# Kernel optimization log

Measured on AMD Instinct MI355X. Metric: run time of the kernel, lower is better.

The kernel has to match this reference:

```python
import jax, jax.numpy as jnp
import numpy as np

B, L, E, F = 4096, 200, 128, 64
NU = NI = 100000

def setup_inputs() -> dict:
    key = jax.random.key(0)
    ks = jax.random.split(key, 8)
    return {
        "user_ids": jax.random.randint(ks[0], (B,), 0, NU),
        "item_ids": jax.random.randint(ks[1], (B, L), 0, NI),
        "features": jax.random.normal(ks[2], (B, L, F), dtype=jnp.float32),
        "user_emb": jax.random.normal(ks[3], (NU, E), dtype=jnp.float32) * 0.1,
        "item_emb": jax.random.normal(ks[4], (NI, E), dtype=jnp.float32) * 0.1,
        "feat_w1": jax.random.normal(ks[5], (E, E + F), dtype=jnp.float32) * (2.0 / (E + F)) ** 0.5,
        "feat_b1": jnp.zeros((E,), jnp.float32),
        "feat_w2": jax.random.normal(ks[6], (E, E), dtype=jnp.float32) * (2.0 / E) ** 0.5,
        "feat_b2": jnp.zeros((E,), jnp.float32),
        "w1": jax.random.normal(ks[7], (E, 3 * E), dtype=jnp.float32) * (2.0 / (3 * E)) ** 0.5,
        "b1": jnp.zeros((E,), jnp.float32),
        "w2": jax.random.normal(jax.random.fold_in(key, 99), (1, E), dtype=jnp.float32) * (2.0 / E) ** 0.5,
        "b2": jnp.zeros((1,), jnp.float32),
    }

def reference(user_ids, item_ids, features, user_emb, item_emb,
              feat_w1, feat_b1, feat_w2, feat_b2, w1, b1, w2, b2):
    user = user_emb[user_ids]                      # [B, E]
    items = item_emb[item_ids]                     # [B, L, E]
    usern = jnp.broadcast_to(user[:, None, :], items.shape)  # [B, L, E]
    # FeatureNet: concat(user, features) -> Linear -> relu -> Linear -> relu
    fx = jnp.concatenate([usern, features], axis=-1)           # [B, L, E+F]
    fx = jax.nn.relu(jnp.einsum('blf,ef->ble', fx, feat_w1) + feat_b1)
    comp = jax.nn.relu(jnp.einsum('ble,oe->blo', fx, feat_w2) + feat_b2)  # [B, L, E]
    # attention MLP over concat(user, item, comp)
    x = jnp.concatenate([usern, items, comp], axis=-1)         # [B, L, 3E]
    x = jax.nn.relu(jnp.einsum('blf,ef->ble', x, w1) + b1)
    logits = jnp.einsum('ble,oe->blo', x, w2) + b2             # [B, L, 1]
    attn = jax.nn.softmax(logits, axis=1)                      # softmax over items
    out = user + jnp.sum(items * attn, axis=1)                 # [B, E]
    return out
```

## Files before the change

kernel.cpp:

```cpp
#include <hip/hip_runtime.h>
#include <math.h>

#define BB 4096
#define LL 200
#define EE 128
#define FF 64
#define NTHREADS 512

#define PITCH_F  72
#define PITCH_FX 136
#define PITCH_X3 264

typedef __attribute__((ext_vector_type(4))) float  floatx4;
typedef __attribute__((ext_vector_type(8))) short  shortx8;

#define MFMA16(a, b, c) __builtin_amdgcn_mfma_f32_16x16x32_bf16((a), (b), (c), 0, 0, 0)

__device__ __forceinline__ unsigned short f2bf(float f) {
    union { float f; unsigned u; } c; c.f = f;
    return (unsigned short)((c.u + 0x7fffu + ((c.u >> 16) & 1u)) >> 16);
}

__device__ __forceinline__ shortx8 load_bfrag(const float* p) {
    float4 v0 = ((const float4*)p)[0];
    float4 v1 = ((const float4*)p)[1];
    shortx8 r;
    r[0] = (short)f2bf(v0.x); r[1] = (short)f2bf(v0.y);
    r[2] = (short)f2bf(v0.z); r[3] = (short)f2bf(v0.w);
    r[4] = (short)f2bf(v1.x); r[5] = (short)f2bf(v1.y);
    r[6] = (short)f2bf(v1.z); r[7] = (short)f2bf(v1.w);
    return r;
}

__device__ __forceinline__ float waveMax(float v) {
    #pragma unroll
    for (int off = 32; off > 0; off >>= 1)
        v = fmaxf(v, __shfl_xor(v, off, 64));
    return v;
}
__device__ __forceinline__ float waveSum(float v) {
    #pragma unroll
    for (int off = 32; off > 0; off >>= 1)
        v += __shfl_xor(v, off, 64);
    return v;
}

__global__ __launch_bounds__(NTHREADS, 4)
void usernet_mfma(const int* __restrict__ user_ids,
                  const int* __restrict__ item_ids,
                  const float* __restrict__ features,
                  const float* __restrict__ user_emb,
                  const float* __restrict__ item_emb,
                  const float* __restrict__ feat_w1,
                  const float* __restrict__ feat_b1,
                  const float* __restrict__ feat_w2,
                  const float* __restrict__ feat_b2,
                  const float* __restrict__ w1,
                  const float* __restrict__ b1,
                  const float* __restrict__ w2,
                  const float* __restrict__ b2,
                  float* __restrict__ out)
{
    __shared__ __align__(16) unsigned short s_feat[64 * PITCH_F];
    __shared__ __align__(16) unsigned short s_fx  [64 * PITCH_FX];
    __shared__ __align__(16) unsigned short s_x3  [64 * PITCH_X3];
    __shared__ float s_user[EE];
    __shared__ float s_bias1[EE];
    __shared__ float s_bias2[EE];
    __shared__ float s_bias3[EE];
    __shared__ float s_w2[EE];
    __shared__ float s_lp[8][208];
    __shared__ float s_attn[208];
    __shared__ float s_red[12];
    __shared__ float s_part[4][EE];

    const int b    = blockIdx.x;
    const int tid  = threadIdx.x;
    const int lane = tid & 63;
    const int wv   = tid >> 6;
    const int m    = lane & 15;
    const int q    = lane >> 4;
    const int n0   = wv * 16 + m;

    shortx8 B1[2];
    shortx8 B2[4];
    shortx8 B3[8];
    #pragma unroll
    for (int ks = 0; ks < 2; ++ks)
        B1[ks] = load_bfrag(feat_w1 + (size_t)n0 * (EE + FF) + EE + ks * 32 + q * 8);
    #pragma unroll
    for (int ks = 0; ks < 4; ++ks)
        B2[ks] = load_bfrag(feat_w2 + (size_t)n0 * EE + ks * 32 + q * 8);
    #pragma unroll
    for (int ks = 0; ks < 8; ++ks)
        B3[ks] = load_bfrag(w1 + (size_t)n0 * (3 * EE) + EE + ks * 32 + q * 8);

    if (tid < 32) {
        const int uid = user_ids[b];
        ((float4*)s_user)[tid] = ((const float4*)(user_emb + (size_t)uid * EE))[tid];
    }
    if (tid >= 64 && tid < 64 + EE) {
        s_bias2[tid - 64] = feat_b2[tid - 64];
        s_w2[tid - 64]    = w2[tid - 64];
    }
    __syncthreads();

    if (tid < 256) {
        const int e    = tid & (EE - 1);
        const int half = tid >> 7;
        const float* wrow = half ? (w1 + (size_t)e * (3 * EE))
                                 : (feat_w1 + (size_t)e * (EE + FF));
        float acc = 0.f;
        #pragma unroll 8
        for (int k = 0; k < EE; ++k) acc += wrow[k] * s_user[k];
        if (half == 0) s_bias1[e] = acc + feat_b1[e];
        else           s_bias3[e] = acc + b1[e];
    }
    __syncthreads();

    const float bias1_0 = s_bias1[n0];
    const float bias2_0 = s_bias2[n0];
    const float bias3_0 = s_bias3[n0];
    const float w2_0    = s_w2[n0];

    for (int ch = 0; ch < 4; ++ch) {
        const int row0 = ch * 64;
        const int ntl  = (ch < 3) ? 4 : 1;
        const int rows = ntl * 16;

        for (int idx = tid; idx < rows * 16; idx += NTHREADS) {
            const int r = idx >> 4, c4 = idx & 15;
            const int l = row0 + r;
            float4 v = make_float4(0.f, 0.f, 0.f, 0.f);
            if (l < LL) v = ((const float4*)features)[((size_t)b * LL + l) * 16 + c4];
            ushort4 o; o.x = f2bf(v.x); o.y = f2bf(v.y); o.z = f2bf(v.z); o.w = f2bf(v.w);
            *(ushort4*)&s_feat[r * PITCH_F + c4 * 4] = o;
        }
        for (int idx = tid; idx < rows * 32; idx += NTHREADS) {
            const int r = idx >> 5, c4 = idx & 31;
            const int l = row0 + r;
            float4 v = make_float4(0.f, 0.f, 0.f, 0.f);
            if (l < LL) {
                const int id = item_ids[(size_t)b * LL + l];
                v = ((const float4*)item_emb)[(size_t)id * 32 + c4];
            }
            ushort4 o; o.x = f2bf(v.x); o.y = f2bf(v.y); o.z = f2bf(v.z); o.w = f2bf(v.w);
            *(ushort4*)&s_x3[r * PITCH_X3 + c4 * 4] = o;
        }
        __syncthreads();

        for (int mt = 0; mt < ntl; ++mt) {
            floatx4 a0 = {0.f, 0.f, 0.f, 0.f};
            const unsigned short* ap = s_feat + (mt * 16 + m) * PITCH_F + q * 8;
            #pragma unroll
            for (int ks = 0; ks < 2; ++ks) {
                shortx8 af = *(const shortx8*)(ap + ks * 32);
                a0 = MFMA16(af, B1[ks], a0);
            }
            #pragma unroll
            for (int r = 0; r < 4; ++r) {
                const int row = mt * 16 + q * 4 + r;
                float v0 = a0[r] + bias1_0; v0 = v0 > 0.f ? v0 : 0.f;
                s_fx[row * PITCH_FX + n0] = f2bf(v0);
            }
        }
        __syncthreads();

        for (int mt = 0; mt < ntl; ++mt) {
            floatx4 a0 = {0.f, 0.f, 0.f, 0.f};
            const unsigned short* ap = s_fx + (mt * 16 + m) * PITCH_FX + q * 8;
            #pragma unroll
            for (int ks = 0; ks < 4; ++ks) {
                shortx8 af = *(const shortx8*)(ap + ks * 32);
                a0 = MFMA16(af, B2[ks], a0);
            }
            #pragma unroll
            for (int r = 0; r < 4; ++r) {
                const int row = mt * 16 + q * 4 + r;
                float v0 = a0[r] + bias2_0; v0 = v0 > 0.f ? v0 : 0.f;
                s_x3[row * PITCH_X3 + EE + n0] = f2bf(v0);
            }
        }
        __syncthreads();

        for (int mt = 0; mt < ntl; ++mt) {
            floatx4 a0 = {0.f, 0.f, 0.f, 0.f};
            const unsigned short* ap = s_x3 + (mt * 16 + m) * PITCH_X3 + q * 8;
            #pragma unroll
            for (int ks = 0; ks < 8; ++ks) {
                shortx8 af = *(const shortx8*)(ap + ks * 32);
                a0 = MFMA16(af, B3[ks], a0);
            }
            #pragma unroll
            for (int r = 0; r < 4; ++r) {
                float v0 = a0[r] + bias3_0; v0 = v0 > 0.f ? v0 : 0.f;
                float p = v0 * w2_0;
                p += __shfl_xor(p, 1, 64);
                p += __shfl_xor(p, 2, 64);
                p += __shfl_xor(p, 4, 64);
                p += __shfl_xor(p, 8, 64);
                if (m == 0) s_lp[wv][row0 + mt * 16 + q * 4 + r] = p;
            }
        }
        __syncthreads();
    }

    const int wid = tid >> 6;
    float lv = -INFINITY;
    if (tid < LL) {
        lv = b2[0];
        #pragma unroll
        for (int w = 0; w < 8; ++w) lv += s_lp[w][tid];
    }
    {
        float mx = waveMax(lv);
        if ((tid & 63) == 0) s_red[wid] = mx;
        __syncthreads();
        if (tid == 0) {
            float g = s_red[0];
            #pragma unroll
            for (int w = 1; w < 8; ++w) g = fmaxf(g, s_red[w]);
            s_red[8] = g;
        }
        __syncthreads();
    }
    const float gmax = s_red[8];
    __syncthreads();
    float ex = (tid < LL) ? __expf(lv - gmax) : 0.f;
    {
        float s = waveSum(ex);
        if ((tid & 63) == 0) s_red[wid] = s;
        __syncthreads();
        if (tid == 0) {
            float g = 0.f;
            #pragma unroll
            for (int w = 0; w < 8; ++w) g += s_red[w];
            s_red[8] = g;
        }
        __syncthreads();
    }
    const float inv = 1.f / s_red[8];
    if (tid < LL) s_attn[tid] = ex * inv;
    __syncthreads();

    {
        const int e = tid & (EE - 1);
        const int g = tid >> 7;
        float acc = 0.f;
        const int lstart = g * (LL / 4);
        for (int l = lstart; l < lstart + LL / 4; ++l) {
            const float a  = s_attn[l];
            const int  id  = item_ids[(size_t)b * LL + l];
            acc += a * item_emb[(size_t)id * EE + e];
        }
        s_part[g][e] = acc;
        __syncthreads();
        if (tid < EE)
            out[(size_t)b * EE + tid] = s_user[tid] + s_part[0][tid] + s_part[1][tid]
                                      + s_part[2][tid] + s_part[3][tid];
    }
}

extern "C" void kernel_launch(void* const* d_in, const int* in_sizes, int n_in,
                              void* d_out, int out_size, void* d_ws, size_t ws_size,
                              hipStream_t stream) {
    const int*   user_ids = (const int*)  d_in[0];
    const int*   item_ids = (const int*)  d_in[1];
    const float* features = (const float*)d_in[2];
    const float* user_emb = (const float*)d_in[3];
    const float* item_emb = (const float*)d_in[4];
    const float* feat_w1  = (const float*)d_in[5];
    const float* feat_b1  = (const float*)d_in[6];
    const float* feat_w2  = (const float*)d_in[7];
    const float* feat_b2  = (const float*)d_in[8];
    const float* w1       = (const float*)d_in[9];
    const float* b1       = (const float*)d_in[10];
    const float* w2       = (const float*)d_in[11];
    const float* b2       = (const float*)d_in[12];
    float* out = (float*)d_out;

    usernet_mfma<<<BB, NTHREADS, 0, stream>>>(user_ids, item_ids, features,
                                              user_emb, item_emb,
                                              feat_w1, feat_b1, feat_w2, feat_b2,
                                              w1, b1, w2, b2, out);
}
```

Measured before the change: 766.0 us.

## Halve row chunk size, raise occupancy target, use packed bf16 conversion

Row chunks shrink from 64 to 32 rows (7 chunks), cutting shared memory per block so more blocks can be resident per CU. The launch-bounds occupancy hint rises from 4 to 8. Per-chunk logit partials are now reduced into a separate logit buffer at the start of the next chunk, and the b2 offset is dropped because softmax ignores a constant shift. Float-to-bf16 rounding now uses the hardware v_cvt_pk_bf16_f32 instruction, converting two values per instruction instead of integer rounding math. The risks are register pressure from the tighter occupancy hint, with the preloaded weight fragments possibly spilling, and nearly twice as many barriers per block.

```diff
diff --git a/kernel.cpp b/kernel.cpp
--- a/kernel.cpp
+++ b/kernel.cpp
@@ -7,6 +7,9 @@
 #define FF 64
 #define NTHREADS 512
 
+#define CROWS 32
+#define NCH 7
+
 #define PITCH_F  72
 #define PITCH_FX 136
 #define PITCH_X3 264
@@ -16,20 +19,30 @@
 
 #define MFMA16(a, b, c) __builtin_amdgcn_mfma_f32_16x16x32_bf16((a), (b), (c), 0, 0, 0)
 
+__device__ __forceinline__ unsigned cvt_pk_bf16(float lo, float hi) {
+    unsigned r;
+    asm("v_cvt_pk_bf16_f32 %0, %1, %2" : "=v"(r) : "v"(lo), "v"(hi));
+    return r;
+}
 __device__ __forceinline__ unsigned short f2bf(float f) {
-    union { float f; unsigned u; } c; c.f = f;
-    return (unsigned short)((c.u + 0x7fffu + ((c.u >> 16) & 1u)) >> 16);
+    return (unsigned short)cvt_pk_bf16(f, f);
+}
+__device__ __forceinline__ uint2 pk4(float4 v) {
+    uint2 o;
+    o.x = cvt_pk_bf16(v.x, v.y);
+    o.y = cvt_pk_bf16(v.z, v.w);
+    return o;
 }
 
 __device__ __forceinline__ shortx8 load_bfrag(const float* p) {
     float4 v0 = ((const float4*)p)[0];
     float4 v1 = ((const float4*)p)[1];
-    shortx8 r;
-    r[0] = (short)f2bf(v0.x); r[1] = (short)f2bf(v0.y);
-    r[2] = (short)f2bf(v0.z); r[3] = (short)f2bf(v0.w);
-    r[4] = (short)f2bf(v1.x); r[5] = (short)f2bf(v1.y);
-    r[6] = (short)f2bf(v1.z); r[7] = (short)f2bf(v1.w);
-    return r;
+    union { unsigned u[4]; shortx8 s; } r;
+    r.u[0] = cvt_pk_bf16(v0.x, v0.y);
+    r.u[1] = cvt_pk_bf16(v0.z, v0.w);
+    r.u[2] = cvt_pk_bf16(v1.x, v1.y);
+    r.u[3] = cvt_pk_bf16(v1.z, v1.w);
+    return r.s;
 }
 
 __device__ __forceinline__ float waveMax(float v) {
@@ -45,7 +58,7 @@
     return v;
 }
 
-__global__ __launch_bounds__(NTHREADS, 4)
+__global__ __launch_bounds__(NTHREADS, 8)
 void usernet_mfma(const int* __restrict__ user_ids,
                   const int* __restrict__ item_ids,
                   const float* __restrict__ features,
@@ -61,15 +74,16 @@
                   const float* __restrict__ b2,
                   float* __restrict__ out)
 {
-    __shared__ __align__(16) unsigned short s_feat[64 * PITCH_F];
-    __shared__ __align__(16) unsigned short s_fx  [64 * PITCH_FX];
-    __shared__ __align__(16) unsigned short s_x3  [64 * PITCH_X3];
+    __shared__ __align__(16) unsigned short s_feat[CROWS * PITCH_F];
+    __shared__ __align__(16) unsigned short s_fx  [CROWS * PITCH_FX];
+    __shared__ __align__(16) unsigned short s_x3  [CROWS * PITCH_X3];
     __shared__ float s_user[EE];
     __shared__ float s_bias1[EE];
     __shared__ float s_bias2[EE];
     __shared__ float s_bias3[EE];
     __shared__ float s_w2[EE];
-    __shared__ float s_lp[8][208];
+    __shared__ float s_lp[8][CROWS];
+    __shared__ float s_logit[208];
     __shared__ float s_attn[208];
     __shared__ float s_red[12];
     __shared__ float s_part[4][EE];
@@ -123,18 +137,24 @@
     const float bias3_0 = s_bias3[n0];
     const float w2_0    = s_w2[n0];
 
-    for (int ch = 0; ch < 4; ++ch) {
-        const int row0 = ch * 64;
-        const int ntl  = (ch < 3) ? 4 : 1;
+    for (int ch = 0; ch < NCH; ++ch) {
+        const int row0 = ch * CROWS;
+        const int ntl  = (ch < NCH - 1) ? 2 : 1;
         const int rows = ntl * 16;
+
+        if (ch > 0 && tid < CROWS) {
+            float p = 0.f;
+            #pragma unroll
+            for (int w = 0; w < 8; ++w) p += s_lp[w][tid];
+            s_logit[row0 - CROWS + tid] = p;
+        }
 
         for (int idx = tid; idx < rows * 16; idx += NTHREADS) {
             const int r = idx >> 4, c4 = idx & 15;
             const int l = row0 + r;
             float4 v = make_float4(0.f, 0.f, 0.f, 0.f);
             if (l < LL) v = ((const float4*)features)[((size_t)b * LL + l) * 16 + c4];
-            ushort4 o; o.x = f2bf(v.x); o.y = f2bf(v.y); o.z = f2bf(v.z); o.w = f2bf(v.w);
-            *(ushort4*)&s_feat[r * PITCH_F + c4 * 4] = o;
+            *(uint2*)&s_feat[r * PITCH_F + c4 * 4] = pk4(v);
         }
         for (int idx = tid; idx < rows * 32; idx += NTHREADS) {
             const int r = idx >> 5, c4 = idx & 31;
@@ -144,8 +164,7 @@
                 const int id = item_ids[(size_t)b * LL + l];
                 v = ((const float4*)item_emb)[(size_t)id * 32 + c4];
             }
-            ushort4 o; o.x = f2bf(v.x); o.y = f2bf(v.y); o.z = f2bf(v.z); o.w = f2bf(v.w);
-            *(ushort4*)&s_x3[r * PITCH_X3 + c4 * 4] = o;
+            *(uint2*)&s_x3[r * PITCH_X3 + c4 * 4] = pk4(v);
         }
         __syncthreads();
 
@@ -199,19 +218,22 @@
                 p += __shfl_xor(p, 2, 64);
                 p += __shfl_xor(p, 4, 64);
                 p += __shfl_xor(p, 8, 64);
-                if (m == 0) s_lp[wv][row0 + mt * 16 + q * 4 + r] = p;
-            }
-        }
-        __syncthreads();
-    }
+                if (m == 0) s_lp[wv][mt * 16 + q * 4 + r] = p;
+            }
+        }
+        __syncthreads();
+    }
+
+    if (tid < 16) {
+        float p = 0.f;
+        #pragma unroll
+        for (int w = 0; w < 8; ++w) p += s_lp[w][tid];
+        s_logit[(NCH - 1) * CROWS + tid] = p;
+    }
+    __syncthreads();
 
     const int wid = tid >> 6;
-    float lv = -INFINITY;
-    if (tid < LL) {
-        lv = b2[0];
-        #pragma unroll
-        for (int w = 0; w < 8; ++w) lv += s_lp[w][tid];
-    }
+    float lv = (tid < LL) ? s_logit[tid] : -INFINITY;
     {
         float mx = waveMax(lv);
         if ((tid & 63) == 0) s_red[wid] = mx;
```

New measurement: 932.8 us. +21.8%, slower.
